# Performance work log

Hardware: AMD Instinct MI355X
Metric: run time of the kernel (lower is better)

## Reference

```python
import jax, jax.numpy as jnp
import numpy as np

NC, NQ, BOX = 20, 27, 6  # classes, queries-per-class, 3D box dim (cx,cy,cz,w,h,d)
COST_CLASS, COST_BBOX, COST_GIOU = 2.0, 5.0, 2.0


def box_cxcyczwhd_to_xyzxyz(b):
    c, s = b[..., :3], b[..., 3:]
    return jnp.concatenate([c - 0.5 * s, c + 0.5 * s], axis=-1)


def giou3d_vs_single(pred, tgt):
    # pred: [B,NC,NQ,6] xyzxyz, tgt: [B,NC,6] xyzxyz -> giou [B,NC,NQ]
    vol_p = jnp.prod(pred[..., 3:] - pred[..., :3], -1)            # [B,NC,NQ]
    vol_t = jnp.prod(tgt[..., 3:] - tgt[..., :3], -1)[..., None]   # [B,NC,1]
    t = tgt[..., None, :]                                          # [B,NC,1,6]
    lt = jnp.maximum(pred[..., :3], t[..., :3])
    rb = jnp.minimum(pred[..., 3:], t[..., 3:])
    inter = jnp.prod(jnp.clip(rb - lt, 0.0), -1)                   # [B,NC,NQ]
    union = vol_p + vol_t - inter
    iou = inter / union
    lt2 = jnp.minimum(pred[..., :3], t[..., :3])
    rb2 = jnp.maximum(pred[..., 3:], t[..., 3:])
    hull = jnp.prod(jnp.clip(rb2 - lt2, 0.0), -1)
    return iou - (hull - union) / hull


def setup_inputs() -> dict:
    key = jax.random.key(0)
    k1, k2, k3, k4 = jax.random.split(key, 4)
    bs = 8192
    return {
        "pred_logits": jax.random.normal(k1, (bs, NC * NQ, 1), dtype=jnp.float32),
        "pred_boxes": jax.random.uniform(k2, (bs, NC * NQ, BOX), dtype=jnp.float32),
        "tgt_boxes": jax.random.uniform(k3, (bs, NC, BOX), dtype=jnp.float32),
        "tgt_present": jax.random.randint(k4, (bs, NC), 0, 2, dtype=jnp.int32),
        "num_top_queries": 1,
    }


def reference(pred_logits, pred_boxes, tgt_boxes, tgt_present, num_top_queries):
    bs = pred_logits.shape[0]
    boxes = pred_boxes.reshape(bs, NC, NQ, BOX).astype(jnp.float32)
    logits = pred_logits.reshape(bs, NC, NQ).astype(jnp.float32)

    cost_class = -jax.nn.sigmoid(logits)                                   # [B,NC,NQ]
    cost_bbox = jnp.sum(jnp.abs(boxes - tgt_boxes[:, :, None, :]), -1)      # L1 cdist, [B,NC,NQ]
    giou = giou3d_vs_single(box_cxcyczwhd_to_xyzxyz(jnp.clip(boxes, 0.0)),
                            box_cxcyczwhd_to_xyzxyz(tgt_boxes))
    cost_giou = -giou                                                       # [B,NC,NQ]

    C = COST_BBOX * cost_bbox + COST_CLASS * cost_class + COST_GIOU * cost_giou

    _, idx = jax.lax.top_k(-C, num_top_queries)                             # smallest-k, [B,NC,k]
    onehot = jax.nn.one_hot(idx, NQ, dtype=jnp.int32).sum(-2)               # [B,NC,NQ]
    present = tgt_present.astype(bool)[..., None]                           # [B,NC,1]
    matches = jnp.where(present, (onehot > 0).astype(jnp.int32), 0)

    gmax = cost_giou.max(-1, keepdims=True)
    gmin = cost_giou.min(-1, keepdims=True)
    soft = jnp.clip((cost_giou - gmax) / (gmin - gmax), 0.0)
    soft_labels = jnp.where(present, soft, -1.0)
    return matches, soft_labels
```

## Files before the change

### kernel.cpp

```cpp
#include <hip/hip_runtime.h>
#include <hip/hip_bf16.h>
#include <math.h>

#define NCC 20
#define NQQ 27
#define BSZ 8192
#define NPAIR (BSZ * NCC)

struct Tgt {
    float tc0, tc1, tc2, tw, th, td;
    float tl0, tl1, tl2, th0, th1, th2, vol;
};

__device__ __forceinline__ Tgt make_tgt(float2 t01, float2 t23, float2 t45) {
    Tgt T;
    T.tc0 = t01.x; T.tc1 = t01.y; T.tc2 = t23.x;
    T.tw  = t23.y; T.th  = t45.x; T.td  = t45.y;
    T.tl0 = T.tc0 - 0.5f * T.tw; T.tl1 = T.tc1 - 0.5f * T.th; T.tl2 = T.tc2 - 0.5f * T.td;
    T.th0 = T.tc0 + 0.5f * T.tw; T.th1 = T.tc1 + 0.5f * T.th; T.th2 = T.tc2 + 0.5f * T.td;
    T.vol = (T.th0 - T.tl0) * (T.th1 - T.tl1) * (T.th2 - T.tl2);
    return T;
}

__device__ __forceinline__ float pair_cost(float2 b01, float2 b23, float2 b45,
                                           float lg, const Tgt& T, float* cg) {
    const float bc0 = b01.x, bc1 = b01.y, bc2 = b23.x;
    const float bw  = b23.y, bh  = b45.x, bd  = b45.y;

    const float cost_class = -1.0f / (1.0f + __expf(-lg));

    const float cost_bbox =
        fabsf(bc0 - T.tc0) + fabsf(bc1 - T.tc1) + fabsf(bc2 - T.tc2) +
        fabsf(bw  - T.tw ) + fabsf(bh  - T.th ) + fabsf(bd  - T.td );

    const float cc0 = fmaxf(bc0, 0.0f), cc1 = fmaxf(bc1, 0.0f), cc2 = fmaxf(bc2, 0.0f);
    const float cw  = fmaxf(bw , 0.0f), ch  = fmaxf(bh , 0.0f), cd  = fmaxf(bd , 0.0f);
    const float pl0 = cc0 - 0.5f * cw, pl1 = cc1 - 0.5f * ch, pl2 = cc2 - 0.5f * cd;
    const float ph0 = cc0 + 0.5f * cw, ph1 = cc1 + 0.5f * ch, ph2 = cc2 + 0.5f * cd;
    const float vol_p = (ph0 - pl0) * (ph1 - pl1) * (ph2 - pl2);

    const float i0 = fmaxf(fminf(ph0, T.th0) - fmaxf(pl0, T.tl0), 0.0f);
    const float i1 = fmaxf(fminf(ph1, T.th1) - fmaxf(pl1, T.tl1), 0.0f);
    const float i2 = fmaxf(fminf(ph2, T.th2) - fmaxf(pl2, T.tl2), 0.0f);
    const float inter = i0 * i1 * i2;
    const float uni   = vol_p + T.vol - inter;
    const float iou   = inter / uni;

    const float h0 = fmaxf(fmaxf(ph0, T.th0) - fminf(pl0, T.tl0), 0.0f);
    const float h1 = fmaxf(fmaxf(ph1, T.th1) - fminf(pl1, T.tl1), 0.0f);
    const float h2 = fmaxf(fmaxf(ph2, T.th2) - fminf(pl2, T.tl2), 0.0f);
    const float hull = h0 * h1 * h2;

    const float giou = iou - (hull - uni) / hull;
    *cg = -giou;
    return 5.0f * cost_bbox + 2.0f * cost_class + 2.0f * (-giou);
}

__global__ __launch_bounds__(256, 5) void matcher_kernel(
    const float* __restrict__ logits,
    const float* __restrict__ boxes,
    const float* __restrict__ tboxes,
    const int*   __restrict__ present,
    float* __restrict__ out_matches,
    float* __restrict__ out_soft)
{
    const int tid = blockIdx.x * blockDim.x + threadIdx.x;
    const int g   = tid >> 5;
    const int q   = tid & 31;
    const int p0  = g * 2;
    const int p1  = p0 + 1;
    const bool valid = (q < NQQ);
    const int qc = valid ? q : (NQQ - 1);

    const float* bq0 = boxes + (size_t)p0 * (NQQ * 6) + qc * 6;
    const float* bq1 = boxes + (size_t)p1 * (NQQ * 6) + qc * 6;
    float2 a01 = *reinterpret_cast<const float2*>(bq0 + 0);
    float2 a23 = *reinterpret_cast<const float2*>(bq0 + 2);
    float2 a45 = *reinterpret_cast<const float2*>(bq0 + 4);
    float2 c01 = *reinterpret_cast<const float2*>(bq1 + 0);
    float2 c23 = *reinterpret_cast<const float2*>(bq1 + 2);
    float2 c45 = *reinterpret_cast<const float2*>(bq1 + 4);
    const float lg0 = logits[(size_t)p0 * NQQ + qc];
    const float lg1 = logits[(size_t)p1 * NQQ + qc];
    const float* t0 = tboxes + (size_t)p0 * 6;
    const float* t1 = tboxes + (size_t)p1 * 6;
    float2 t0a = *reinterpret_cast<const float2*>(t0 + 0);
    float2 t0b = *reinterpret_cast<const float2*>(t0 + 2);
    float2 t0c = *reinterpret_cast<const float2*>(t0 + 4);
    float2 t1a = *reinterpret_cast<const float2*>(t1 + 0);
    float2 t1b = *reinterpret_cast<const float2*>(t1 + 2);
    float2 t1c = *reinterpret_cast<const float2*>(t1 + 4);
    const int pres0 = present[p0];
    const int pres1 = present[p1];

    const Tgt T0 = make_tgt(t0a, t0b, t0c);
    const Tgt T1 = make_tgt(t1a, t1b, t1c);

    float cg0, cg1;
    float C0 = pair_cost(a01, a23, a45, lg0, T0, &cg0);
    float C1 = pair_cost(c01, c23, c45, lg1, T1, &cg1);
    if (!valid) { C0 = INFINITY; C1 = INFINITY; }

    float m0 = C0, m1 = C1;
    float gx0 = valid ? cg0 : -INFINITY, gn0 = valid ? cg0 : INFINITY;
    float gx1 = valid ? cg1 : -INFINITY, gn1 = valid ? cg1 : INFINITY;
#pragma unroll
    for (int s = 16; s >= 1; s >>= 1) {
        m0  = fminf(m0,  __shfl_xor(m0,  s, 32));
        m1  = fminf(m1,  __shfl_xor(m1,  s, 32));
        gx0 = fmaxf(gx0, __shfl_xor(gx0, s, 32));
        gn0 = fminf(gn0, __shfl_xor(gn0, s, 32));
        gx1 = fmaxf(gx1, __shfl_xor(gx1, s, 32));
        gn1 = fminf(gn1, __shfl_xor(gn1, s, 32));
    }
    const unsigned long long b0 = __ballot(C0 == m0);
    const unsigned long long b1 = __ballot(C1 == m1);
    const int shift = (threadIdx.x & 32);
    const unsigned int g0 = (unsigned int)(b0 >> shift);
    const unsigned int g1 = (unsigned int)(b1 >> shift);
    const int idx0 = __ffs(g0) - 1;
    const int idx1 = __ffs(g1) - 1;

    if (valid) {
        const float s0 = fmaxf((cg0 - gx0) / (gn0 - gx0), 0.0f);
        const float s1 = fmaxf((cg1 - gx1) / (gn1 - gx1), 0.0f);
        out_matches[(size_t)p0 * NQQ + q] = (pres0 && q == idx0) ? 1.0f : 0.0f;
        out_matches[(size_t)p1 * NQQ + q] = (pres1 && q == idx1) ? 1.0f : 0.0f;
        out_soft   [(size_t)p0 * NQQ + q] = pres0 ? s0 : -1.0f;
        out_soft   [(size_t)p1 * NQQ + q] = pres1 ? s1 : -1.0f;
    }
}

extern "C" void kernel_launch(void* const* d_in, const int* in_sizes, int n_in,
                              void* d_out, int out_size, void* d_ws, size_t ws_size,
                              hipStream_t stream) {
    const float* logits  = (const float*)d_in[0];
    const float* boxes   = (const float*)d_in[1];
    const float* tboxes  = (const float*)d_in[2];
    const int*   presnt  = (const int*)d_in[3];

    float* out = (float*)d_out;
    float* out_matches = out;
    float* out_soft    = out + (size_t)NPAIR * NQQ;

    const int total_threads = (NPAIR / 2) * 32;
    dim3 block(256);
    dim3 grid(total_threads / 256);
    matcher_kernel<<<grid, block, 0, stream>>>(logits, boxes, tboxes, presnt,
                                               out_matches, out_soft);
}
```

Measured before the change: 35.68 us.

## Map each pair to 8 lanes with 4 queries per lane

Thread mapping changes from 32 lanes per two (batch,class) pairs to 8 lanes per pair, each lane computing 4 queries. The per-pair target setup is no longer repeated across many lanes, lanes are no longer idle on padding (27 of 32 were used before), and the shuffle reduction drops from 5 to 3 steps. The cost is strided per-lane loads (stride of 4 boxes) that coalesce less well, more registers per thread, and scattered 4-element stores. It also changes how the division is done, using a reciprocal multiply instead of two divides.

```diff
diff --git a/kernel.cpp b/kernel.cpp
--- a/kernel.cpp
+++ b/kernel.cpp
@@ -65,70 +65,86 @@
     float* __restrict__ out_soft)
 {
     const int tid = blockIdx.x * blockDim.x + threadIdx.x;
-    const int g   = tid >> 5;
-    const int q   = tid & 31;
-    const int p0  = g * 2;
-    const int p1  = p0 + 1;
-    const bool valid = (q < NQQ);
-    const int qc = valid ? q : (NQQ - 1);
+    const int p   = tid >> 3;
+    const int l   = tid & 7;
+    const int q0  = l * 4;
 
-    const float* bq0 = boxes + (size_t)p0 * (NQQ * 6) + qc * 6;
-    const float* bq1 = boxes + (size_t)p1 * (NQQ * 6) + qc * 6;
-    float2 a01 = *reinterpret_cast<const float2*>(bq0 + 0);
-    float2 a23 = *reinterpret_cast<const float2*>(bq0 + 2);
-    float2 a45 = *reinterpret_cast<const float2*>(bq0 + 4);
-    float2 c01 = *reinterpret_cast<const float2*>(bq1 + 0);
-    float2 c23 = *reinterpret_cast<const float2*>(bq1 + 2);
-    float2 c45 = *reinterpret_cast<const float2*>(bq1 + 4);
-    const float lg0 = logits[(size_t)p0 * NQQ + qc];
-    const float lg1 = logits[(size_t)p1 * NQQ + qc];
-    const float* t0 = tboxes + (size_t)p0 * 6;
-    const float* t1 = tboxes + (size_t)p1 * 6;
-    float2 t0a = *reinterpret_cast<const float2*>(t0 + 0);
-    float2 t0b = *reinterpret_cast<const float2*>(t0 + 2);
-    float2 t0c = *reinterpret_cast<const float2*>(t0 + 4);
-    float2 t1a = *reinterpret_cast<const float2*>(t1 + 0);
-    float2 t1b = *reinterpret_cast<const float2*>(t1 + 2);
-    float2 t1c = *reinterpret_cast<const float2*>(t1 + 4);
-    const int pres0 = present[p0];
-    const int pres1 = present[p1];
+    const int qa = (q0 + 0 < NQQ) ? q0 + 0 : NQQ - 1;
+    const int qb = (q0 + 1 < NQQ) ? q0 + 1 : NQQ - 1;
+    const int qc = (q0 + 2 < NQQ) ? q0 + 2 : NQQ - 1;
+    const int qd = (q0 + 3 < NQQ) ? q0 + 3 : NQQ - 1;
 
-    const Tgt T0 = make_tgt(t0a, t0b, t0c);
-    const Tgt T1 = make_tgt(t1a, t1b, t1c);
+    const float* bp = boxes + (size_t)p * (NQQ * 6);
+    float2 a01 = *reinterpret_cast<const float2*>(bp + qa * 6 + 0);
+    float2 a23 = *reinterpret_cast<const float2*>(bp + qa * 6 + 2);
+    float2 a45 = *reinterpret_cast<const float2*>(bp + qa * 6 + 4);
+    float2 b01 = *reinterpret_cast<const float2*>(bp + qb * 6 + 0);
+    float2 b23 = *reinterpret_cast<const float2*>(bp + qb * 6 + 2);
+    float2 b45 = *reinterpret_cast<const float2*>(bp + qb * 6 + 4);
+    float2 c01 = *reinterpret_cast<const float2*>(bp + qc * 6 + 0);
+    float2 c23 = *reinterpret_cast<const float2*>(bp + qc * 6 + 2);
+    float2 c45 = *reinterpret_cast<const float2*>(bp + qc * 6 + 4);
+    float2 d01 = *reinterpret_cast<const float2*>(bp + qd * 6 + 0);
+    float2 d23 = *reinterpret_cast<const float2*>(bp + qd * 6 + 2);
+    float2 d45 = *reinterpret_cast<const float2*>(bp + qd * 6 + 4);
+    const float* lp = logits + (size_t)p * NQQ;
+    const float lga = lp[qa], lgb = lp[qb], lgc = lp[qc], lgd = lp[qd];
+    const float* t = tboxes + (size_t)p * 6;
+    float2 t01 = *reinterpret_cast<const float2*>(t + 0);
+    float2 t23 = *reinterpret_cast<const float2*>(t + 2);
+    float2 t45 = *reinterpret_cast<const float2*>(t + 4);
+    const int pres = present[p];
 
-    float cg0, cg1;
-    float C0 = pair_cost(a01, a23, a45, lg0, T0, &cg0);
-    float C1 = pair_cost(c01, c23, c45, lg1, T1, &cg1);
-    if (!valid) { C0 = INFINITY; C1 = INFINITY; }
+    const Tgt T = make_tgt(t01, t23, t45);
 
-    float m0 = C0, m1 = C1;
-    float gx0 = valid ? cg0 : -INFINITY, gn0 = valid ? cg0 : INFINITY;
-    float gx1 = valid ? cg1 : -INFINITY, gn1 = valid ? cg1 : INFINITY;
+    const bool va = (q0 + 0 < NQQ), vb = (q0 + 1 < NQQ),
+               vc = (q0 + 2 < NQQ), vd = (q0 + 3 < NQQ);
+
+    float cg0, cg1, cg2, cg3;
+    float C0 = pair_cost(a01, a23, a45, lga, T, &cg0);
+    float C1 = pair_cost(b01, b23, b45, lgb, T, &cg1);
+    float C2 = pair_cost(c01, c23, c45, lgc, T, &cg2);
+    float C3 = pair_cost(d01, d23, d45, lgd, T, &cg3);
+    if (!va) C0 = INFINITY;
+    if (!vb) C1 = INFINITY;
+    if (!vc) C2 = INFINITY;
+    if (!vd) C3 = INFINITY;
+
+    float bestC = C0; int bestj = 0;
+    if (C1 < bestC) { bestC = C1; bestj = 1; }
+    if (C2 < bestC) { bestC = C2; bestj = 2; }
+    if (C3 < bestC) { bestC = C3; bestj = 3; }
+    float gx = va ? cg0 : -INFINITY;
+    float gn = va ? cg0 :  INFINITY;
+    if (vb) { gx = fmaxf(gx, cg1); gn = fminf(gn, cg1); }
+    if (vc) { gx = fmaxf(gx, cg2); gn = fminf(gn, cg2); }
+    if (vd) { gx = fmaxf(gx, cg3); gn = fminf(gn, cg3); }
+
+    float m = bestC;
 #pragma unroll
-    for (int s = 16; s >= 1; s >>= 1) {
-        m0  = fminf(m0,  __shfl_xor(m0,  s, 32));
-        m1  = fminf(m1,  __shfl_xor(m1,  s, 32));
-        gx0 = fmaxf(gx0, __shfl_xor(gx0, s, 32));
-        gn0 = fminf(gn0, __shfl_xor(gn0, s, 32));
-        gx1 = fmaxf(gx1, __shfl_xor(gx1, s, 32));
-        gn1 = fminf(gn1, __shfl_xor(gn1, s, 32));
+    for (int s = 4; s >= 1; s >>= 1) {
+        m  = fminf(m,  __shfl_xor(m,  s, 8));
+        gx = fmaxf(gx, __shfl_xor(gx, s, 8));
+        gn = fminf(gn, __shfl_xor(gn, s, 8));
     }
-    const unsigned long long b0 = __ballot(C0 == m0);
-    const unsigned long long b1 = __ballot(C1 == m1);
-    const int shift = (threadIdx.x & 32);
-    const unsigned int g0 = (unsigned int)(b0 >> shift);
-    const unsigned int g1 = (unsigned int)(b1 >> shift);
-    const int idx0 = __ffs(g0) - 1;
-    const int idx1 = __ffs(g1) - 1;
 
-    if (valid) {
-        const float s0 = fmaxf((cg0 - gx0) / (gn0 - gx0), 0.0f);
-        const float s1 = fmaxf((cg1 - gx1) / (gn1 - gx1), 0.0f);
-        out_matches[(size_t)p0 * NQQ + q] = (pres0 && q == idx0) ? 1.0f : 0.0f;
-        out_matches[(size_t)p1 * NQQ + q] = (pres1 && q == idx1) ? 1.0f : 0.0f;
-        out_soft   [(size_t)p0 * NQQ + q] = pres0 ? s0 : -1.0f;
-        out_soft   [(size_t)p1 * NQQ + q] = pres1 ? s1 : -1.0f;
-    }
+    const unsigned long long bal = __ballot(bestC == m);
+    const int gbase  = (threadIdx.x & 63) & ~7;
+    const unsigned int gbits = (unsigned int)(bal >> gbase) & 0xFFu;
+    const int winner = __ffs(gbits) - 1;
+    const bool mine  = (winner == l);
+
+    float* om = out_matches + (size_t)p * NQQ + q0;
+    float* os = out_soft    + (size_t)p * NQQ + q0;
+    const float inv = 1.0f / (gn - gx);
+    if (va) { om[0] = (pres && mine && bestj == 0) ? 1.0f : 0.0f;
+              os[0] = pres ? fmaxf((cg0 - gx) * inv, 0.0f) : -1.0f; }
+    if (vb) { om[1] = (pres && mine && bestj == 1) ? 1.0f : 0.0f;
+              os[1] = pres ? fmaxf((cg1 - gx) * inv, 0.0f) : -1.0f; }
+    if (vc) { om[2] = (pres && mine && bestj == 2) ? 1.0f : 0.0f;
+              os[2] = pres ? fmaxf((cg2 - gx) * inv, 0.0f) : -1.0f; }
+    if (vd) { om[3] = (pres && mine && bestj == 3) ? 1.0f : 0.0f;
+              os[3] = pres ? fmaxf((cg3 - gx) * inv, 0.0f) : -1.0f; }
 }
 
 extern "C" void kernel_launch(void* const* d_in, const int* in_sizes, int n_in,
@@ -143,9 +159,8 @@
     float* out_matches = out;
     float* out_soft    = out + (size_t)NPAIR * NQQ;
 
-    const int total_threads = (NPAIR / 2) * 32;
     dim3 block(256);
-    dim3 grid(total_threads / 256);
+    dim3 grid((NPAIR * 8) / 256);
     matcher_kernel<<<grid, block, 0, stream>>>(logits, boxes, tboxes, presnt,
                                                out_matches, out_soft);
 }
```

Result: no change. 36.04 us (+1.0%).
